# Optimization experiments

Measured on AMD Instinct MI355X. Metric: run time of the kernel, lower is better.

Reference implementation:

```python
import jax, jax.numpy as jnp
import numpy as np

E = 1024      # embed_dim
H = 16        # num heads
D = E // H    # head_dim = 64
B, T = 4, 2048


def setup_inputs() -> dict:
    key = jax.random.key(0)
    ks = jax.random.split(key, 7)
    hidden_states = jax.random.normal(ks[0], (B, T, E), dtype=jnp.float32)
    # torch Linear weight layout: [out_features, in_features]
    Wqkv = jax.random.normal(ks[1], (3 * E, E), dtype=jnp.float32) * (1.0 / np.sqrt(E))
    bqkv = jax.random.normal(ks[2], (3 * E,), dtype=jnp.float32) * 0.02
    Wproj = jax.random.normal(ks[3], (E, E), dtype=jnp.float32) * (1.0 / np.sqrt(E))
    bproj = jax.random.normal(ks[4], (E,), dtype=jnp.float32) * 0.02
    splat_scale = jax.random.normal(ks[5], (H,), dtype=jnp.float32) * 0.5
    splat_bias = jax.random.normal(ks[6], (H, 1, 1), dtype=jnp.float32) * 0.5
    return {
        'hidden_states': hidden_states,
        'Wqkv': Wqkv, 'bqkv': bqkv,
        'Wproj': Wproj, 'bproj': bproj,
        'splat_scale': splat_scale, 'splat_bias': splat_bias,
    }


def reference(hidden_states, Wqkv, bqkv, Wproj, bproj, splat_scale, splat_bias):
    b, t, _ = hidden_states.shape
    scale_factor = 1.0 / np.sqrt(D)

    qkv = hidden_states @ Wqkv.T + bqkv                    # [B,T,3E]
    q, k, v = jnp.split(qkv, 3, axis=-1)
    # [B,H,T,D]
    q = q.reshape(b, t, H, D).transpose(0, 2, 1, 3)
    k = k.reshape(b, t, H, D).transpose(0, 2, 1, 3)
    v = v.reshape(b, t, H, D).transpose(0, 2, 1, 3)

    scores = jnp.einsum('bhqd,bhkd->bhqk', q * scale_factor, k)  # [B,H,T,T]

    s = (1.0 + 0.01 * jnp.tanh(splat_scale)).reshape(1, H, 1, 1)
    bsp = (0.001 * jnp.tanh(splat_bias)).reshape(1, H, 1, 1)
    scores = s * scores + bsp

    causal = jnp.tril(jnp.ones((t, t), dtype=bool))
    scores = jnp.where(causal, scores, jnp.float32(-1e9))

    attn = jax.nn.softmax(scores, axis=-1)                 # dropout = identity (eval)
    out = jnp.einsum('bhqk,bhkd->bhqd', attn, v)
    out = out.transpose(0, 2, 1, 3).reshape(b, t, E)
    out = out @ Wproj.T + bproj
    return out
```

## Files before the change

### kernel.cpp

```cpp
#include <hip/hip_runtime.h>
#include <stdint.h>

#define BB 4
#define TT 2048
#define EE 1024
#define HH 16
#define DD 64
#define MM (BB*TT)
#define NQKV (3*EE)

typedef __bf16 bf16_t;
typedef bf16_t bf16x8 __attribute__((ext_vector_type(8)));
typedef float floatx4 __attribute__((ext_vector_type(4)));

__device__ __forceinline__ unsigned short f2bf(float f) {
    unsigned int u = __float_as_uint(f);
    u = (u + 0x7FFFu + ((u >> 16) & 1u)) >> 16;
    return (unsigned short)u;
}

__device__ __forceinline__ void load_lds16(const void* g, void* l) {
    __builtin_amdgcn_global_load_lds(
        (const __attribute__((address_space(1))) unsigned int*)g,
        (__attribute__((address_space(3))) unsigned int*)l, 16, 0, 0);
}

__global__ void cvt_f32_bf16(const float* __restrict__ in,
                             unsigned short* __restrict__ out, int n) {
    int i = (blockIdx.x * 256 + threadIdx.x) * 4;
    if (i + 3 < n) {
        float4 v = *reinterpret_cast<const float4*>(in + i);
        ushort4 o;
        o.x = f2bf(v.x); o.y = f2bf(v.y); o.z = f2bf(v.z); o.w = f2bf(v.w);
        *reinterpret_cast<ushort4*>(out + i) = o;
    }
}

template<int N, int K, int EPI>
__global__ __launch_bounds__(256, 2) void gemm_bt(
    const unsigned short* __restrict__ A,
    const unsigned short* __restrict__ Bw,
    const float* __restrict__ bias,
    const float* __restrict__ sscale,
    unsigned short* __restrict__ Qb,
    unsigned short* __restrict__ Kb,
    unsigned short* __restrict__ Vtb,
    float* __restrict__ Cout)
{
    __shared__ __align__(16) unsigned short As[128 * 32];
    __shared__ __align__(16) unsigned short Bs[128 * 32];
    __shared__ float qsc[16];

    const int tid  = threadIdx.x;
    const int lane = tid & 63;
    const int w    = tid >> 6;
    const int quad = lane >> 4;
    const int l16  = lane & 15;
    const int m0   = blockIdx.y * 128;
    const int n0   = blockIdx.x * 128;
    const int wm   = (w & 1) * 64;
    const int wn   = (w >> 1) * 64;

    if (EPI == 0 && tid < 16) qsc[tid] = (1.0f + 0.01f * tanhf(sscale[tid])) * 0.125f;

    floatx4 acc[4][4] = {};

    for (int kk = 0; kk < K; kk += 32) {
        __syncthreads();
#pragma unroll
        for (int c = 0; c < 2; ++c) {
            int idx = c * 256 + tid;
            const unsigned short* ga = A  + (size_t)(m0 + (idx >> 2)) * K + kk + (idx & 3) * 8;
            load_lds16(ga, &As[(c * 256 + w * 64) * 8]);
            const unsigned short* gb = Bw + (size_t)(n0 + (idx >> 2)) * K + kk + (idx & 3) * 8;
            load_lds16(gb, &Bs[(c * 256 + w * 64) * 8]);
        }
        __syncthreads();

        bf16x8 af[4], bfr[4];
#pragma unroll
        for (int mt = 0; mt < 4; ++mt)
            af[mt] = *reinterpret_cast<const bf16x8*>(&As[(wm + mt * 16 + l16) * 32 + quad * 8]);
#pragma unroll
        for (int nt = 0; nt < 4; ++nt)
            bfr[nt] = *reinterpret_cast<const bf16x8*>(&Bs[(wn + nt * 16 + l16) * 32 + quad * 8]);
#pragma unroll
        for (int mt = 0; mt < 4; ++mt)
#pragma unroll
            for (int nt = 0; nt < 4; ++nt)
                acc[mt][nt] = __builtin_amdgcn_mfma_f32_16x16x32_bf16(af[mt], bfr[nt], acc[mt][nt], 0, 0, 0);
    }

    if (EPI == 0) {
#pragma unroll
        for (int mt = 0; mt < 4; ++mt) {
            int rowb = m0 + wm + mt * 16 + quad * 4;
#pragma unroll
            for (int nt = 0; nt < 4; ++nt) {
                int col = n0 + wn + nt * 16 + l16;
                int which = col >> 10;
                int e = col & 1023;
                int h = e >> 6, d = e & 63;
                float bsv = bias[col];
#pragma unroll
                for (int r = 0; r < 4; ++r) {
                    int m = rowb + r;
                    int b = m >> 11, t = m & 2047;
                    float v = acc[mt][nt][r] + bsv;
                    size_t bh = (size_t)(b * HH + h);
                    if (which == 0) {
                        v *= qsc[h];
                        Qb[(bh * TT + t) * DD + d] = f2bf(v);
                    } else if (which == 1) {
                        Kb[(bh * TT + t) * DD + d] = f2bf(v);
                    } else {
                        Vtb[(bh * DD + d) * TT + t] = f2bf(v);
                    }
                }
            }
        }
    } else {
#pragma unroll
        for (int mt = 0; mt < 4; ++mt) {
            int rowb = m0 + wm + mt * 16 + quad * 4;
#pragma unroll
            for (int nt = 0; nt < 4; ++nt) {
                int col = n0 + wn + nt * 16 + l16;
                float bsv = bias[col];
#pragma unroll
                for (int r = 0; r < 4; ++r)
                    Cout[(size_t)(rowb + r) * N + col] = acc[mt][nt][r] + bsv;
            }
        }
    }
}

#define LP 72
__global__ __launch_bounds__(256, 3) void flash_attn(
    const unsigned short* __restrict__ Qb,
    const unsigned short* __restrict__ Kb,
    const unsigned short* __restrict__ Vtb,
    unsigned short* __restrict__ Ob)
{
    __shared__ __align__(16) unsigned short Ks[64 * LP];
    __shared__ __align__(16) unsigned short Vs[64 * LP];
    __shared__ __align__(16) unsigned short Ps[128 * LP];

    const int tid  = threadIdx.x;
    const int lane = tid & 63;
    const int w    = tid >> 6;
    const int quad = lane >> 4;
    const int l16  = lane & 15;
    const int bh   = blockIdx.y;
    const int qt   = 15 - blockIdx.x;
    const int row0 = qt * 128 + w * 32;

    bf16x8 qf[2][2];
#pragma unroll
    for (int mt = 0; mt < 2; ++mt)
#pragma unroll
        for (int kh = 0; kh < 2; ++kh)
            qf[mt][kh] = *reinterpret_cast<const bf16x8*>(
                &Qb[((size_t)bh * TT + row0 + mt * 16 + l16) * DD + kh * 32 + quad * 8]);

    const bf16x8 vones = { (bf16_t)1.0f, (bf16_t)1.0f, (bf16_t)1.0f, (bf16_t)1.0f,
                           (bf16_t)1.0f, (bf16_t)1.0f, (bf16_t)1.0f, (bf16_t)1.0f };

    floatx4 o[2][4] = {};
    floatx4 o1[2] = {};

    const int ktmax = 2 * qt + 1;
    for (int kt = 0; kt <= ktmax; ++kt) {
        __syncthreads();
#pragma unroll
        for (int c = 0; c < 2; ++c) {
            int idx = c * 256 + tid;
            int rr = idx >> 3, cc = (idx & 7) * 8;
            uint4 kv = *reinterpret_cast<const uint4*>(
                &Kb[((size_t)bh * TT + kt * 64 + rr) * DD + cc]);
            *reinterpret_cast<uint4*>(&Ks[rr * LP + cc]) = kv;
            uint4 vv = *reinterpret_cast<const uint4*>(
                &Vtb[((size_t)bh * DD + rr) * TT + kt * 64 + cc]);
            *reinterpret_cast<uint4*>(&Vs[rr * LP + cc]) = vv;
        }
        __syncthreads();

        if (kt * 64 <= row0 + 31) {
            floatx4 s[2][4];
#pragma unroll
            for (int mt = 0; mt < 2; ++mt)
#pragma unroll
                for (int nt = 0; nt < 4; ++nt)
                    s[mt][nt] = floatx4{0.f, 0.f, 0.f, 0.f};
#pragma unroll
            for (int kh = 0; kh < 2; ++kh) {
#pragma unroll
                for (int nt = 0; nt < 4; ++nt) {
                    bf16x8 kf = *reinterpret_cast<const bf16x8*>(
                        &Ks[(nt * 16 + l16) * LP + kh * 32 + quad * 8]);
#pragma unroll
                    for (int mt = 0; mt < 2; ++mt)
                        s[mt][nt] = __builtin_amdgcn_mfma_f32_16x16x32_bf16(
                            qf[mt][kh], kf, s[mt][nt], 0, 0, 0);
                }
            }

            if (kt >= 2 * qt) {
#pragma unroll
                for (int nt = 0; nt < 4; ++nt) {
                    int key = kt * 64 + nt * 16 + l16;
#pragma unroll
                    for (int mt = 0; mt < 2; ++mt) {
                        int rowb = row0 + mt * 16 + quad * 4;
#pragma unroll
                        for (int r = 0; r < 4; ++r)
                            if (key > rowb + r) s[mt][nt][r] = -1e30f;
                    }
                }
            }

#pragma unroll
            for (int mt = 0; mt < 2; ++mt)
#pragma unroll
                for (int nt = 0; nt < 4; ++nt)
#pragma unroll
                    for (int r = 0; r < 4; ++r) {
                        float p = __expf(s[mt][nt][r]);
                        Ps[(w * 32 + mt * 16 + quad * 4 + r) * LP + nt * 16 + l16] = f2bf(p);
                    }

#pragma unroll
            for (int kh = 0; kh < 2; ++kh) {
                bf16x8 pf[2];
#pragma unroll
                for (int mt = 0; mt < 2; ++mt) {
                    pf[mt] = *reinterpret_cast<const bf16x8*>(
                        &Ps[(w * 32 + mt * 16 + l16) * LP + kh * 32 + quad * 8]);
                    o1[mt] = __builtin_amdgcn_mfma_f32_16x16x32_bf16(
                        pf[mt], vones, o1[mt], 0, 0, 0);
                }
#pragma unroll
                for (int dt = 0; dt < 4; ++dt) {
                    bf16x8 vf = *reinterpret_cast<const bf16x8*>(
                        &Vs[(dt * 16 + l16) * LP + kh * 32 + quad * 8]);
#pragma unroll
                    for (int mt = 0; mt < 2; ++mt)
                        o[mt][dt] = __builtin_amdgcn_mfma_f32_16x16x32_bf16(
                            pf[mt], vf, o[mt][dt], 0, 0, 0);
                }
            }
        }
    }

    const int b = bh >> 4, h = bh & 15;
#pragma unroll
    for (int mt = 0; mt < 2; ++mt) {
#pragma unroll
        for (int r = 0; r < 4; ++r) {
            int q = row0 + mt * 16 + quad * 4 + r;
            float rl = __builtin_amdgcn_rcpf(o1[mt][r]);
#pragma unroll
            for (int dt = 0; dt < 4; ++dt)
                Ob[((size_t)(b * TT + q)) * EE + h * DD + dt * 16 + l16] =
                    f2bf(o[mt][dt][r] * rl);
        }
    }
}

extern "C" void kernel_launch(void* const* d_in, const int* in_sizes, int n_in,
                              void* d_out, int out_size, void* d_ws, size_t ws_size,
                              hipStream_t stream) {
    const float* hs    = (const float*)d_in[0];
    const float* Wqkv  = (const float*)d_in[1];
    const float* bqkv  = (const float*)d_in[2];
    const float* Wproj = (const float*)d_in[3];
    const float* bproj = (const float*)d_in[4];
    const float* ss    = (const float*)d_in[5];
    float* out = (float*)d_out;

    char* p = (char*)d_ws;
    unsigned short* hsb    = (unsigned short*)p; p += (size_t)MM * EE * 2;
    unsigned short* wqkvb  = (unsigned short*)p; p += (size_t)NQKV * EE * 2;
    unsigned short* wprojb = (unsigned short*)p; p += (size_t)EE * EE * 2;
    unsigned short* Qb     = (unsigned short*)p; p += (size_t)BB*HH*TT*DD * 2;
    unsigned short* Kb     = (unsigned short*)p; p += (size_t)BB*HH*TT*DD * 2;
    unsigned short* Vtb    = (unsigned short*)p; p += (size_t)BB*HH*TT*DD * 2;

    cvt_f32_bf16<<<(MM * EE) / 1024, 256, 0, stream>>>(hs, hsb, MM * EE);
    cvt_f32_bf16<<<(NQKV * EE) / 1024, 256, 0, stream>>>(Wqkv, wqkvb, NQKV * EE);
    cvt_f32_bf16<<<(EE * EE) / 1024, 256, 0, stream>>>(Wproj, wprojb, EE * EE);

    gemm_bt<NQKV, EE, 0><<<dim3(NQKV / 128, MM / 128), 256, 0, stream>>>(
        hsb, wqkvb, bqkv, ss, Qb, Kb, Vtb, nullptr);

    flash_attn<<<dim3(TT / 128, BB * HH), 256, 0, stream>>>(Qb, Kb, Vtb, hsb);

    gemm_bt<EE, EE, 1><<<dim3(EE / 128, MM / 128), 256, 0, stream>>>(
        hsb, wprojb, bproj, nullptr, nullptr, nullptr, nullptr, out);
}
```

Baseline: 328.4 us.

## Keep P in registers via transposed QK^T and double-buffer K/V tiles

Computes S^T by swapping the MFMA operands so each lane's exp'd probabilities already sit in the A-operand layout of a 16x16x16 bf16 MFMA. The P matrix no longer goes through LDS, removing the Ps buffer and its store/load round trip. K/V tiles are now prefetched into registers one iteration ahead and written to double-buffered LDS, which drops one barrier per iteration. The causal mask is applied as a select to zero after exp instead of -inf before it. The change also raises the occupancy target to 4 blocks, which could increase register pressure and spills. Using the smaller K=16 MFMA doubles the instruction count for the PV product.

```diff
diff --git a/kernel.cpp b/kernel.cpp
--- a/kernel.cpp
+++ b/kernel.cpp
@@ -11,7 +11,8 @@
 
 typedef __bf16 bf16_t;
 typedef bf16_t bf16x8 __attribute__((ext_vector_type(8)));
-typedef float floatx4 __attribute__((ext_vector_type(4)));
+typedef short  s16x4  __attribute__((ext_vector_type(4)));
+typedef float  floatx4 __attribute__((ext_vector_type(4)));
 
 __device__ __forceinline__ unsigned short f2bf(float f) {
     unsigned int u = __float_as_uint(f);
@@ -136,15 +137,14 @@
 }
 
 #define LP 72
-__global__ __launch_bounds__(256, 3) void flash_attn(
+__global__ __launch_bounds__(256, 4) void flash_attn(
     const unsigned short* __restrict__ Qb,
     const unsigned short* __restrict__ Kb,
     const unsigned short* __restrict__ Vtb,
     unsigned short* __restrict__ Ob)
 {
-    __shared__ __align__(16) unsigned short Ks[64 * LP];
-    __shared__ __align__(16) unsigned short Vs[64 * LP];
-    __shared__ __align__(16) unsigned short Ps[128 * LP];
+    __shared__ __align__(16) unsigned short Ks[2][64 * LP];
+    __shared__ __align__(16) unsigned short Vs[2][64 * LP];
 
     const int tid  = threadIdx.x;
     const int lane = tid & 63;
@@ -163,89 +163,89 @@
             qf[mt][kh] = *reinterpret_cast<const bf16x8*>(
                 &Qb[((size_t)bh * TT + row0 + mt * 16 + l16) * DD + kh * 32 + quad * 8]);
 
-    const bf16x8 vones = { (bf16_t)1.0f, (bf16_t)1.0f, (bf16_t)1.0f, (bf16_t)1.0f,
-                           (bf16_t)1.0f, (bf16_t)1.0f, (bf16_t)1.0f, (bf16_t)1.0f };
+    const s16x4 vones = { (short)0x3F80, (short)0x3F80, (short)0x3F80, (short)0x3F80 };
 
     floatx4 o[2][4] = {};
     floatx4 o1[2] = {};
 
     const int ktmax = 2 * qt + 1;
+
+    uint4 kreg[2], vreg[2];
+#pragma unroll
+    for (int c = 0; c < 2; ++c) {
+        int idx = c * 256 + tid;
+        int rr = idx >> 3, cc = (idx & 7) * 8;
+        kreg[c] = *reinterpret_cast<const uint4*>(&Kb[((size_t)bh * TT + rr) * DD + cc]);
+        vreg[c] = *reinterpret_cast<const uint4*>(&Vtb[((size_t)bh * DD + rr) * TT + cc]);
+    }
+
     for (int kt = 0; kt <= ktmax; ++kt) {
-        __syncthreads();
+        const int buf = kt & 1;
 #pragma unroll
         for (int c = 0; c < 2; ++c) {
             int idx = c * 256 + tid;
             int rr = idx >> 3, cc = (idx & 7) * 8;
-            uint4 kv = *reinterpret_cast<const uint4*>(
-                &Kb[((size_t)bh * TT + kt * 64 + rr) * DD + cc]);
-            *reinterpret_cast<uint4*>(&Ks[rr * LP + cc]) = kv;
-            uint4 vv = *reinterpret_cast<const uint4*>(
-                &Vtb[((size_t)bh * DD + rr) * TT + kt * 64 + cc]);
-            *reinterpret_cast<uint4*>(&Vs[rr * LP + cc]) = vv;
+            *reinterpret_cast<uint4*>(&Ks[buf][rr * LP + cc]) = kreg[c];
+            *reinterpret_cast<uint4*>(&Vs[buf][rr * LP + cc]) = vreg[c];
         }
         __syncthreads();
 
+        if (kt < ktmax) {
+#pragma unroll
+            for (int c = 0; c < 2; ++c) {
+                int idx = c * 256 + tid;
+                int rr = idx >> 3, cc = (idx & 7) * 8;
+                kreg[c] = *reinterpret_cast<const uint4*>(
+                    &Kb[((size_t)bh * TT + (kt + 1) * 64 + rr) * DD + cc]);
+                vreg[c] = *reinterpret_cast<const uint4*>(
+                    &Vtb[((size_t)bh * DD + rr) * TT + (kt + 1) * 64 + cc]);
+            }
+        }
+
         if (kt * 64 <= row0 + 31) {
-            floatx4 s[2][4];
-#pragma unroll
-            for (int mt = 0; mt < 2; ++mt)
-#pragma unroll
-                for (int nt = 0; nt < 4; ++nt)
-                    s[mt][nt] = floatx4{0.f, 0.f, 0.f, 0.f};
+            floatx4 st[4][2];
+#pragma unroll
+            for (int ntk = 0; ntk < 4; ++ntk)
+#pragma unroll
+                for (int mt = 0; mt < 2; ++mt)
+                    st[ntk][mt] = floatx4{0.f, 0.f, 0.f, 0.f};
 #pragma unroll
             for (int kh = 0; kh < 2; ++kh) {
 #pragma unroll
-                for (int nt = 0; nt < 4; ++nt) {
+                for (int ntk = 0; ntk < 4; ++ntk) {
                     bf16x8 kf = *reinterpret_cast<const bf16x8*>(
-                        &Ks[(nt * 16 + l16) * LP + kh * 32 + quad * 8]);
+                        &Ks[buf][(ntk * 16 + l16) * LP + kh * 32 + quad * 8]);
 #pragma unroll
                     for (int mt = 0; mt < 2; ++mt)
-                        s[mt][nt] = __builtin_amdgcn_mfma_f32_16x16x32_bf16(
-                            qf[mt][kh], kf, s[mt][nt], 0, 0, 0);
+                        st[ntk][mt] = __builtin_amdgcn_mfma_f32_16x16x32_bf16(
+                            kf, qf[mt][kh], st[ntk][mt], 0, 0, 0);
                 }
             }
 
-            if (kt >= 2 * qt) {
-#pragma unroll
-                for (int nt = 0; nt < 4; ++nt) {
-                    int key = kt * 64 + nt * 16 + l16;
-#pragma unroll
-                    for (int mt = 0; mt < 2; ++mt) {
-                        int rowb = row0 + mt * 16 + quad * 4;
-#pragma unroll
-                        for (int r = 0; r < 4; ++r)
-                            if (key > rowb + r) s[mt][nt][r] = -1e30f;
+            const int keyb = kt * 64 + quad * 4;
+            const int qr0  = row0 + l16;
+#pragma unroll
+            for (int ntk = 0; ntk < 4; ++ntk) {
+                s16x4 pf[2];
+#pragma unroll
+                for (int mt = 0; mt < 2; ++mt) {
+#pragma unroll
+                    for (int r = 0; r < 4; ++r) {
+                        float p = __expf(st[ntk][mt][r]);
+                        int key = keyb + ntk * 16 + r;
+                        p = (key <= qr0 + mt * 16) ? p : 0.0f;
+                        pf[mt][r] = (short)f2bf(p);
                     }
-                }
-            }
-
-#pragma unroll
-            for (int mt = 0; mt < 2; ++mt)
-#pragma unroll
-                for (int nt = 0; nt < 4; ++nt)
-#pragma unroll
-                    for (int r = 0; r < 4; ++r) {
-                        float p = __expf(s[mt][nt][r]);
-                        Ps[(w * 32 + mt * 16 + quad * 4 + r) * LP + nt * 16 + l16] = f2bf(p);
-                    }
-
-#pragma unroll
-            for (int kh = 0; kh < 2; ++kh) {
-                bf16x8 pf[2];
-#pragma unroll
-                for (int mt = 0; mt < 2; ++mt) {
-                    pf[mt] = *reinterpret_cast<const bf16x8*>(
-                        &Ps[(w * 32 + mt * 16 + l16) * LP + kh * 32 + quad * 8]);
-                    o1[mt] = __builtin_amdgcn_mfma_f32_16x16x32_bf16(
+                    o1[mt] = __builtin_amdgcn_mfma_f32_16x16x16bf16_1k(
                         pf[mt], vones, o1[mt], 0, 0, 0);
                 }
 #pragma unroll
                 for (int dt = 0; dt < 4; ++dt) {
-                    bf16x8 vf = *reinterpret_cast<const bf16x8*>(
-                        &Vs[(dt * 16 + l16) * LP + kh * 32 + quad * 8]);
+                    s16x4 vf = *reinterpret_cast<const s16x4*>(
+                        &Vs[buf][(dt * 16 + l16) * LP + ntk * 16 + quad * 4]);
 #pragma unroll
                     for (int mt = 0; mt < 2; ++mt)
-                        o[mt][dt] = __builtin_amdgcn_mfma_f32_16x16x32_bf16(
+                        o[mt][dt] = __builtin_amdgcn_mfma_f32_16x16x16bf16_1k(
                             pf[mt], vf, o[mt][dt], 0, 0, 0);
                 }
             }
```

Result: slower. 406.6 us (+23.8%).
